# Kernel tuning notes

Hardware: AMD Instinct MI355X
Metric: run time of the kernel (lower is better)

Reference implementation:

```python
import jax, jax.numpy as jnp
import numpy as np

B, T, N, DIN, H, E, K, HM, CH, HOR, DOUT = 64, 12, 307, 1, 64, 10, 2, 16, 14, 12, 1
EPS = 1e-12


def setup_inputs() -> dict:
    key = jax.random.key(0)
    ks = jax.random.split(key, 16)
    rn = lambda k, s, sc=0.1: jax.random.normal(k, s, dtype=jnp.float32) * sc
    return {
        "hyper_source": jax.random.normal(ks[0], (B, CH, T, N), dtype=jnp.float32),
        "source": jax.random.normal(ks[1], (B, T, N, DIN), dtype=jnp.float32),
        "adj": jax.random.uniform(ks[2], (N, N), dtype=jnp.float32),
        "node_embeddings": rn(ks[3], (N, E), 1.0),
        "main_weights_pool": rn(ks[4], (E, H, DIN)),
        "hyper_W": rn(ks[5], (CH, H)),
        "hyper_b": jnp.zeros((H,), jnp.float32),
        "mask_W1": rn(ks[6], (H, HM)),
        "mask_W2": rn(ks[7], (HM, E)),
        "gate_Wpool": rn(ks[8], (E, K, 2 * DIN + H, 2 * H)),
        "gate_bpool": rn(ks[9], (E, 2 * H)),
        "upd_Wpool": rn(ks[10], (E, K, 2 * DIN + H, H)),
        "upd_bpool": rn(ks[11], (E, H)),
        "ln_gamma": jnp.ones((H,), jnp.float32),
        "ln_beta": jnp.zeros((H,), jnp.float32),
        "end_W": rn(ks[12], (HOR * DOUT, H)),
        "end_b": jnp.zeros((HOR * DOUT,), jnp.float32),
    }


def _forward(hyper_source, source, adj, node_embeddings, main_weights_pool,
             hyper_W, hyper_b, mask_W1, mask_W2, gate_Wpool, gate_bpool,
             upd_Wpool, upd_bpool, ln_gamma, ln_beta, end_W, end_b):
    # HyperNet: chunked long-history signal -> per-node per-step hidden h [B,N,T,H]
    h = jnp.tanh(jnp.einsum('bctn,ch->bnth', hyper_source, hyper_W) + hyper_b)
    # adaptive input channel: einsum('bnld,ndi->blni') with per-node weights
    weights_h = jnp.einsum('nd,dhi->nhi', node_embeddings, main_weights_pool)  # [N,H,DIN]
    x_adapt = jnp.einsum('bnlh,nhi->blni', h, weights_h)                       # [B,T,N,DIN]
    x = jnp.concatenate([x_adapt, source], axis=-1)                            # [B,T,N,2*DIN]
    # static Chebyshev supports (cheb_k=2): identity + mix(normalized adj, adaptive graph)
    adj_n = adj / jnp.clip(adj.sum(-1, keepdims=True), 1e-6)
    adapt = jax.nn.softmax(jax.nn.relu(node_embeddings @ node_embeddings.T), axis=1)
    A = 0.5 * (adj_n + adapt)
    supports = jnp.stack([jnp.eye(N, dtype=x.dtype), A])                       # [K,N,N]
    # per-node graph-conv weights generated from node embeddings
    gate_W = jnp.einsum('nd,dkio->nkio', node_embeddings, gate_Wpool)
    gate_b = node_embeddings @ gate_bpool
    upd_W = jnp.einsum('nd,dkio->nkio', node_embeddings, upd_Wpool)
    upd_b = node_embeddings @ upd_bpool

    def gconv(sup_b, xin, Wn, bn):
        xg = jnp.einsum('bknm,bmi->bnki', sup_b, xin)
        return jnp.einsum('bnki,nkio->bno', xg, Wn) + bn

    def step(state, inp):
        xt, ht = inp  # [B,N,2*DIN], [B,N,H]
        # dynamic graph sparsification mask from hypernet state
        logits = jnp.einsum('bne,me->bnm', (ht @ mask_W1) @ mask_W2, node_embeddings)
        mask = jax.nn.sigmoid(logits)                # [B,N,N]
        sup_b = supports[None] * mask[:, None]       # [B,K,N,N]
        xs = jnp.concatenate([xt, state], axis=-1)
        zr = jax.nn.sigmoid(gconv(sup_b, xs, gate_W, gate_b))
        z, r = jnp.split(zr, 2, axis=-1)
        cand = jnp.concatenate([xt, z * state], axis=-1)
        hc = jnp.tanh(gconv(sup_b, cand, upd_W, upd_b))
        return r * state + (1.0 - r) * hc, None

    init = jnp.zeros((x.shape[0], N, H), x.dtype)
    state, _ = jax.lax.scan(step, init,
                            (jnp.swapaxes(x, 0, 1), jnp.transpose(h, (2, 0, 1, 3))))
    # layernorm(eps=1e-12); dropout is identity at eval
    mu = state.mean(-1, keepdims=True)
    var = ((state - mu) ** 2).mean(-1, keepdims=True)
    xn = (state - mu) / jnp.sqrt(var + EPS) * ln_gamma + ln_beta
    # end_conv: Conv2d(1, HOR*DOUT, kernel=(1,H)) == per-node linear H -> HOR*DOUT
    out = jnp.einsum('bnh,oh->bon', xn, end_W) + end_b[None, :, None]
    out = out.reshape(-1, HOR, DOUT, N).transpose(0, 1, 3, 2)  # [B,HOR,N,DOUT]
    return out


def reference(hyper_source, source, adj, node_embeddings, main_weights_pool,
              hyper_W, hyper_b, mask_W1, mask_W2, gate_Wpool, gate_bpool,
              upd_Wpool, upd_bpool, ln_gamma, ln_beta, end_W, end_b):
    return _forward(hyper_source, source, adj, node_embeddings, main_weights_pool,
                    hyper_W, hyper_b, mask_W1, mask_W2, gate_Wpool, gate_bpool,
                    upd_Wpool, upd_bpool, ln_gamma, ln_beta, end_W, end_b)
```

## Files before the change

kernel.cpp:

```cpp
#include <hip/hip_runtime.h>
#include <hip/hip_bf16.h>

#define N_ 307
#define B_ 64
#define T_ 12
#define H_ 64
#define E_ 10
#define CH_ 14
#define HM_ 16
#define I2_ 66
#define GO_ 128
#define UO_ 64
#define QG_ (2 * I2_ * GO_)
#define QU_ (2 * I2_ * UO_)
#define TBN_ (T_ * B_ * N_)

__device__ __forceinline__ float wsum(float v) {
    #pragma unroll
    for (int off = 32; off; off >>= 1) v += __shfl_xor(v, off);
    return v;
}
__device__ __forceinline__ float wmax(float v) {
    #pragma unroll
    for (int off = 32; off; off >>= 1) v = fmaxf(v, __shfl_xor(v, off));
    return v;
}
__device__ __forceinline__ float sigm(float x) { return 1.f / (1.f + __expf(-x)); }
__device__ __forceinline__ float ftanh(float x) { return 1.f - 2.f / (__expf(2.f * x) + 1.f); }
__device__ __forceinline__ float bcast(float v, int l) {
    return __int_as_float(__builtin_amdgcn_readlane(__float_as_int(v), l));
}

__global__ void A_kernel(const float* __restrict__ adj, const float* __restrict__ nemb,
                         float* __restrict__ A) {
    const int n = blockIdx.x;
    const int lane = threadIdx.x;
    float en[E_];
    #pragma unroll
    for (int d = 0; d < E_; ++d) en[d] = nemb[n * E_ + d];
    float asum = 0.f;
    for (int m = lane; m < N_; m += 64) asum += adj[n * N_ + m];
    asum = fmaxf(wsum(asum), 1e-6f);
    float g[5]; bool valid[5];
    float mx = -1e30f;
    #pragma unroll
    for (int it = 0; it < 5; ++it) {
        int m = lane + it * 64;
        valid[it] = (m < N_);
        float dt = 0.f;
        if (valid[it]) {
            #pragma unroll
            for (int e = 0; e < E_; ++e) dt += en[e] * nemb[m * E_ + e];
            dt = fmaxf(dt, 0.f);
            mx = fmaxf(mx, dt);
        }
        g[it] = dt;
    }
    mx = wmax(mx);
    float se = 0.f;
    #pragma unroll
    for (int it = 0; it < 5; ++it)
        if (valid[it]) { g[it] = __expf(g[it] - mx); se += g[it]; }
    se = wsum(se);
    float inv = 1.f / se;
    #pragma unroll
    for (int it = 0; it < 5; ++it) {
        int m = lane + it * 64;
        if (valid[it]) A[n * N_ + m] = 0.5f * (adj[n * N_ + m] / asum + g[it] * inv);
    }
}

__device__ __forceinline__ float embdot(const float* __restrict__ nemb, int n,
                                        const float* __restrict__ pool, int Q, int q) {
    float a = 0.f;
    #pragma unroll
    for (int d = 0; d < E_; ++d) a += nemb[n * E_ + d] * pool[d * Q + q];
    return a;
}

__global__ __launch_bounds__(256) void gen_kernel(
    const float* __restrict__ nemb,
    const float* __restrict__ gWp, const float* __restrict__ gbp,
    const float* __restrict__ uWp, const float* __restrict__ ubp,
    const float* __restrict__ mwp,
    const float* __restrict__ W1, const float* __restrict__ W2,
    float* __restrict__ gW, float* __restrict__ gb,
    float* __restrict__ uW, float* __restrict__ ub,
    float* __restrict__ wh_t, float* __restrict__ W12) {
    const int e0 = N_ * QG_;
    const int e1 = e0 + N_ * GO_;
    const int e2 = e1 + N_ * QU_;
    const int e3 = e2 + N_ * UO_;
    const int e4 = e3 + N_ * H_;
    const int e5 = e4 + H_ * E_;
    int idx = blockIdx.x * 256 + threadIdx.x;
    if (idx < e0) {
        int n = idx / QG_, q = idx % QG_;
        gW[idx] = embdot(nemb, n, gWp, QG_, q);
    } else if (idx < e1) {
        int i = idx - e0; int n = i / GO_, q = i % GO_;
        gb[i] = embdot(nemb, n, gbp, GO_, q);
    } else if (idx < e2) {
        int i = idx - e1; int n = i / QU_, q = i % QU_;
        uW[i] = embdot(nemb, n, uWp, QU_, q);
    } else if (idx < e3) {
        int i = idx - e2; int n = i / UO_, q = i % UO_;
        ub[i] = embdot(nemb, n, ubp, UO_, q);
    } else if (idx < e4) {
        int i = idx - e3; int n = i / H_, q = i % H_;
        wh_t[q * N_ + n] = embdot(nemb, n, mwp, H_, q);
    } else if (idx < e5) {
        int i = idx - e4; int j = i / E_, e = i % E_;
        float a = 0.f;
        #pragma unroll
        for (int q = 0; q < HM_; ++q) a += W1[j * HM_ + q] * W2[q * E_ + e];
        W12[i] = a;
    }
}

__global__ __launch_bounds__(256) void hyper2_kernel(
    const float* __restrict__ hs, const float* __restrict__ src,
    const float* __restrict__ hyper_W, const float* __restrict__ hyper_b,
    const float* __restrict__ wh_t, const float* __restrict__ W12,
    float* __restrict__ x0, float* __restrict__ x1, float* __restrict__ emb) {
    const int tb = blockIdx.y;
    const int t = tb / B_, b = tb % B_;
    const int n = blockIdx.x * 256 + threadIdx.x;
    const bool act = (n < N_);
    const int nc = act ? n : N_ - 1;
    float hsv[CH_];
    #pragma unroll
    for (int c = 0; c < CH_; ++c)
        hsv[c] = hs[((b * CH_ + c) * T_ + t) * N_ + nc];
    float ax0 = 0.f;
    float ae[E_] = {};
    #pragma unroll 8
    for (int j = 0; j < H_; ++j) {
        float hj = hyper_b[j];
        #pragma unroll
        for (int c = 0; c < CH_; ++c) hj = fmaf(hsv[c], hyper_W[c * H_ + j], hj);
        hj = ftanh(hj);
        ax0 = fmaf(hj, wh_t[j * N_ + nc], ax0);
        #pragma unroll
        for (int e = 0; e < E_; ++e) ae[e] = fmaf(hj, W12[j * E_ + e], ae[e]);
    }
    if (act) {
        const int tbn = tb * N_ + n;
        x0[tbn] = ax0;
        x1[tbn] = src[(b * T_ + t) * N_ + n];
        #pragma unroll
        for (int e = 0; e < E_; ++e) emb[e * TBN_ + tbn] = ae[e];
    }
}

__global__ __launch_bounds__(256) void wm_kernel(
    const float* __restrict__ A, const float* __restrict__ emb,
    const float* __restrict__ nemb, const float* __restrict__ x0,
    const float* __restrict__ x1, float* __restrict__ Wm,
    float* __restrict__ dmask, float* __restrict__ aggx, int t) {
    const int wid = __builtin_amdgcn_readfirstlane(blockIdx.x * 4 + (threadIdx.x >> 6));
    const int lane = threadIdx.x & 63;
    const int b = wid / N_;
    const int n = wid % N_;
    const int tbn = (t * B_ + b) * N_ + n;
    const int xb = tbn - n;
    float et[E_];
    #pragma unroll
    for (int d = 0; d < E_; ++d) et[d] = emb[(size_t)d * TBN_ + tbn];
    float* wr = Wm + (size_t)(b * N_ + n) * N_;
    float a0 = 0.f, a1 = 0.f;
    #pragma unroll
    for (int c = 0; c < 5; ++c) {
        int m = c * 64 + lane;
        bool v = (m < N_);
        int mc = v ? m : 0;
        float dt = 0.f;
        #pragma unroll
        for (int d = 0; d < E_; ++d) dt += et[d] * nemb[mc * E_ + d];
        float sg = sigm(dt);
        float w = v ? A[n * N_ + mc] * sg : 0.f;
        if (v) {
            wr[m] = w;
            if (m == n) dmask[tbn] = sg;
            a0 += w * x0[xb + mc];
            a1 += w * x1[xb + mc];
        }
    }
    a0 = wsum(a0);
    a1 = wsum(a1);
    if (lane == 0) {
        aggx[(size_t)tbn * 2] = a0;
        aggx[(size_t)tbn * 2 + 1] = a1;
    }
}

__global__ __launch_bounds__(512) void aggS_kernel(
    const float* __restrict__ Wm, const float* __restrict__ Sin,
    float* __restrict__ aggS) {
    __shared__ float s_lds[N_ * 64];
    const int tid = threadIdx.x;
    const int lane = tid & 63;
    const int wv = tid >> 6;
    const int b = blockIdx.y;
    const int nb = blockIdx.x * 32 + wv * 4;
    {
        const float4* s4 = (const float4*)(Sin + (size_t)b * N_ * 64);
        float4* d4 = (float4*)s_lds;
        for (int idx = tid; idx < N_ * 16; idx += 512) d4[idx] = s4[idx];
    }
    __syncthreads();
    int roff[4];
    #pragma unroll
    for (int r = 0; r < 4; ++r) {
        int nr = nb + r; if (nr > N_ - 1) nr = N_ - 1;
        roff[r] = __builtin_amdgcn_readfirstlane((b * N_ + nr) * N_);
    }
    float acc[4] = {0.f, 0.f, 0.f, 0.f};
    #pragma unroll
    for (int ck = 0; ck < 4; ++ck) {
        const int m0 = ck << 6;
        float w0 = Wm[roff[0] + m0 + lane];
        float w1 = Wm[roff[1] + m0 + lane];
        float w2 = Wm[roff[2] + m0 + lane];
        float w3 = Wm[roff[3] + m0 + lane];
        #pragma unroll 8
        for (int mm = 0; mm < 64; ++mm) {
            float sv = s_lds[(m0 + mm) * 64 + lane];
            acc[0] = fmaf(bcast(w0, mm), sv, acc[0]);
            acc[1] = fmaf(bcast(w1, mm), sv, acc[1]);
            acc[2] = fmaf(bcast(w2, mm), sv, acc[2]);
            acc[3] = fmaf(bcast(w3, mm), sv, acc[3]);
        }
    }
    {
        const int m0 = 256;
        bool v = (m0 + lane < N_);
        float w0 = v ? Wm[roff[0] + m0 + lane] : 0.f;
        float w1 = v ? Wm[roff[1] + m0 + lane] : 0.f;
        float w2 = v ? Wm[roff[2] + m0 + lane] : 0.f;
        float w3 = v ? Wm[roff[3] + m0 + lane] : 0.f;
        #pragma unroll 8
        for (int mm = 0; mm < 51; ++mm) {
            float sv = s_lds[(m0 + mm) * 64 + lane];
            acc[0] = fmaf(bcast(w0, mm), sv, acc[0]);
            acc[1] = fmaf(bcast(w1, mm), sv, acc[1]);
            acc[2] = fmaf(bcast(w2, mm), sv, acc[2]);
            acc[3] = fmaf(bcast(w3, mm), sv, acc[3]);
        }
    }
    #pragma unroll
    for (int r = 0; r < 4; ++r) {
        int nr = nb + r;
        if (nr < N_) aggS[((size_t)b * N_ + nr) * 64 + lane] = acc[r];
    }
}

__global__ __launch_bounds__(256) void gate_mm_kernel(
    const float* __restrict__ gate_W, const float* __restrict__ gate_b,
    const float* __restrict__ x0, const float* __restrict__ x1,
    const float* __restrict__ S, const float* __restrict__ dmask,
    const float* __restrict__ aggx, const float* __restrict__ aggS,
    float* __restrict__ zs, float* __restrict__ rbuf, int t) {
    __shared__ float W_s[132][64];
    __shared__ float xg_s[32][132];
    const int oh = blockIdx.x, bh = blockIdx.y, n = blockIdx.z;
    const int tid = threadIdx.x;
    for (int idx = tid; idx < 132 * 64; idx += 256) {
        int row = idx >> 6, op = idx & 63;
        int col = (op < 32) ? (oh * 32 + op) : (64 + oh * 32 + (op - 32));
        W_s[row][op] = gate_W[(n * 132 + row) * GO_ + col];
    }
    for (int idx = tid; idx < 32 * 132; idx += 256) {
        int bl = idx / 132, i = idx % 132;
        int b = bh * 32 + bl;
        int tb = (t * B_ + b) * N_ + n;
        float v;
        if (i < 66) {
            float xs = (i == 0) ? x0[tb] : (i == 1) ? x1[tb] : S[(b * N_ + n) * 64 + (i - 2)];
            v = dmask[tb] * xs;
        } else {
            int i2 = i - 66;
            v = (i2 < 2) ? aggx[(size_t)tb * 2 + i2] : aggS[(b * N_ + n) * 64 + (i2 - 2)];
        }
        xg_s[bl][i] = v;
    }
    __syncthreads();
    const int bl = tid >> 3, og = tid & 7;
    float acc[8] = {};
    for (int i = 0; i < 132; ++i) {
        float xv = xg_s[bl][i];
        #pragma unroll
        for (int r = 0; r < 8; ++r) acc[r] += xv * W_s[i][og * 8 + r];
    }
    float v[8];
    #pragma unroll
    for (int r = 0; r < 8; ++r) {
        int op = og * 8 + r;
        int col = (op < 32) ? (oh * 32 + op) : (64 + oh * 32 + (op - 32));
        v[r] = sigm(acc[r] + gate_b[n * GO_ + col]);
    }
    __syncthreads();
    float* zr_s = &xg_s[0][0];
    #pragma unroll
    for (int r = 0; r < 8; ++r) zr_s[bl * 64 + og * 8 + r] = v[r];
    __syncthreads();
    for (int idx = tid; idx < 32 * 32; idx += 256) {
        int bl2 = idx >> 5, jl = idx & 31;
        int b = bh * 32 + bl2;
        int j = oh * 32 + jl;
        float z = zr_s[bl2 * 64 + jl];
        float rr = zr_s[bl2 * 64 + 32 + jl];
        int sidx = (b * N_ + n) * 64 + j;
        zs[sidx] = z * S[sidx];
        rbuf[sidx] = rr;
    }
}

__global__ __launch_bounds__(256) void upd_mm_kernel(
    const float* __restrict__ upd_W, const float* __restrict__ upd_b,
    const float* __restrict__ x0, const float* __restrict__ x1,
    const float* __restrict__ zsrc, const float* __restrict__ dmask,
    const float* __restrict__ aggx, const float* __restrict__ aggS,
    const float* __restrict__ rbuf, float* __restrict__ S, int t) {
    __shared__ float W_s[132][64];
    __shared__ float xg_s[32][132];
    const int bh = blockIdx.x, n = blockIdx.y;
    const int tid = threadIdx.x;
    for (int idx = tid; idx < 132 * 64; idx += 256) {
        int row = idx >> 6, op = idx & 63;
        W_s[row][op] = upd_W[(n * 132 + row) * UO_ + op];
    }
    for (int idx = tid; idx < 32 * 132; idx += 256) {
        int bl = idx / 132, i = idx % 132;
        int b = bh * 32 + bl;
        int tb = (t * B_ + b) * N_ + n;
        float v;
        if (i < 66) {
            float xs = (i == 0) ? x0[tb] : (i == 1) ? x1[tb] : zsrc[(b * N_ + n) * 64 + (i - 2)];
            v = dmask[tb] * xs;
        } else {
            int i2 = i - 66;
            v = (i2 < 2) ? aggx[(size_t)tb * 2 + i2] : aggS[(b * N_ + n) * 64 + (i2 - 2)];
        }
        xg_s[bl][i] = v;
    }
    __syncthreads();
    const int bl = tid >> 3, og = tid & 7;
    float acc[8] = {};
    for (int i = 0; i < 132; ++i) {
        float xv = xg_s[bl][i];
        #pragma unroll
        for (int r = 0; r < 8; ++r) acc[r] += xv * W_s[i][og * 8 + r];
    }
    const int b = bh * 32 + bl;
    #pragma unroll
    for (int r = 0; r < 8; ++r) {
        int op = og * 8 + r;
        float hc = ftanh(acc[r] + upd_b[n * UO_ + op]);
        int sidx = (b * N_ + n) * 64 + op;
        float rr = rbuf[sidx];
        float sv = S[sidx];
        S[sidx] = rr * sv + (1.f - rr) * hc;
    }
}

__global__ __launch_bounds__(256) void final_kernel(
    const float* __restrict__ S, const float* __restrict__ gamma,
    const float* __restrict__ beta, const float* __restrict__ endW,
    const float* __restrict__ endb, float* __restrict__ out) {
    const int wid = blockIdx.x * 4 + (threadIdx.x >> 6);
    const int lane = threadIdx.x & 63;
    const int b = wid / N_, n = wid % N_;
    float s = S[wid * 64 + lane];
    float mu = wsum(s) * (1.f / 64.f);
    float d = s - mu;
    float var = wsum(d * d) * (1.f / 64.f);
    float xn = d / sqrtf(var + 1e-12f) * gamma[lane] + beta[lane];
    #pragma unroll
    for (int o = 0; o < 12; ++o) {
        float dot = wsum(xn * endW[o * 64 + lane]);
        if (lane == o) out[(b * 12 + o) * N_ + n] = dot + endb[o];
    }
}

extern "C" void kernel_launch(void* const* d_in, const int* in_sizes, int n_in,
                              void* d_out, int out_size, void* d_ws, size_t ws_size,
                              hipStream_t stream) {
    const float* hyper_source = (const float*)d_in[0];
    const float* source       = (const float*)d_in[1];
    const float* adj          = (const float*)d_in[2];
    const float* nemb         = (const float*)d_in[3];
    const float* mwpool       = (const float*)d_in[4];
    const float* hyper_W      = (const float*)d_in[5];
    const float* hyper_b      = (const float*)d_in[6];
    const float* mask_W1      = (const float*)d_in[7];
    const float* mask_W2      = (const float*)d_in[8];
    const float* gate_Wpool   = (const float*)d_in[9];
    const float* gate_bpool   = (const float*)d_in[10];
    const float* upd_Wpool    = (const float*)d_in[11];
    const float* upd_bpool    = (const float*)d_in[12];
    const float* ln_gamma     = (const float*)d_in[13];
    const float* ln_beta      = (const float*)d_in[14];
    const float* end_W        = (const float*)d_in[15];
    const float* end_b        = (const float*)d_in[16];
    float* out = (float*)d_out;

    float* ws = (float*)d_ws;
    size_t off = 0;
    auto alloc = [&](size_t nf) {
        float* p = ws + off;
        off += (nf + 255) & ~(size_t)255;
        return p;
    };
    float* A      = alloc((size_t)N_ * N_);
    float* wh_t   = alloc((size_t)N_ * H_);
    float* W12    = alloc((size_t)H_ * E_);
    float* gate_W = alloc((size_t)N_ * QG_);
    float* gate_b = alloc((size_t)N_ * GO_);
    float* upd_W  = alloc((size_t)N_ * QU_);
    float* upd_b  = alloc((size_t)N_ * UO_);
    float* x0     = alloc((size_t)TBN_);
    float* x1     = alloc((size_t)TBN_);
    float* emb    = alloc((size_t)TBN_ * E_);
    float* dmask  = alloc((size_t)TBN_);
    float* aggx   = alloc((size_t)TBN_ * 2);
    float* S      = alloc((size_t)B_ * N_ * H_);
    float* zs     = alloc((size_t)B_ * N_ * H_);
    float* rbuf   = alloc((size_t)B_ * N_ * H_);
    float* aggS   = alloc((size_t)B_ * N_ * H_);
    float* Wm     = alloc((size_t)B_ * N_ * N_);

    hipMemsetAsync(S, 0, (size_t)B_ * N_ * H_ * sizeof(float), stream);

    A_kernel<<<N_, 64, 0, stream>>>(adj, nemb, A);

    const int gen_total = N_ * QG_ + N_ * GO_ + N_ * QU_ + N_ * UO_ + N_ * H_ + H_ * E_;
    gen_kernel<<<(gen_total + 255) / 256, 256, 0, stream>>>(
        nemb, gate_Wpool, gate_bpool, upd_Wpool, upd_bpool, mwpool, mask_W1, mask_W2,
        gate_W, gate_b, upd_W, upd_b, wh_t, W12);

    hyper2_kernel<<<dim3(2, T_ * B_), 256, 0, stream>>>(hyper_source, source, hyper_W,
                                                        hyper_b, wh_t, W12, x0, x1, emb);

    for (int t = 0; t < T_; ++t) {
        wm_kernel<<<(B_ * N_) / 4, 256, 0, stream>>>(A, emb, nemb, x0, x1, Wm, dmask, aggx, t);
        aggS_kernel<<<dim3(10, B_), 512, 0, stream>>>(Wm, S, aggS);
        gate_mm_kernel<<<dim3(2, 2, N_), 256, 0, stream>>>(gate_W, gate_b, x0, x1, S, dmask,
                                                           aggx, aggS, zs, rbuf, t);
        aggS_kernel<<<dim3(10, B_), 512, 0, stream>>>(Wm, zs, aggS);
        upd_mm_kernel<<<dim3(2, N_), 256, 0, stream>>>(upd_W, upd_b, x0, x1, zs, dmask, aggx,
                                                       aggS, rbuf, S, t);
    }

    final_kernel<<<(B_ * N_) / 4, 256, 0, stream>>>(S, ln_gamma, ln_beta, end_W, end_b, out);
}
```

Baseline: 2.303 ms.

## Store mask-weighted graph matrix in bf16 and retile aggregation and gate/update matmuls

After: 2.623 ms. 13.9% more time.

```diff
diff --git a/kernel.cpp b/kernel.cpp
--- a/kernel.cpp
+++ b/kernel.cpp
@@ -14,6 +14,7 @@
 #define QG_ (2 * I2_ * GO_)
 #define QU_ (2 * I2_ * UO_)
 #define TBN_ (T_ * B_ * N_)
+#define WMP_ 320
 
 __device__ __forceinline__ float wsum(float v) {
     #pragma unroll
@@ -29,6 +30,14 @@
 __device__ __forceinline__ float ftanh(float x) { return 1.f - 2.f / (__expf(2.f * x) + 1.f); }
 __device__ __forceinline__ float bcast(float v, int l) {
     return __int_as_float(__builtin_amdgcn_readlane(__float_as_int(v), l));
+}
+__device__ __forceinline__ unsigned short f2bf(float f) {
+    unsigned u = __float_as_uint(f);
+    u += 0x7FFFu + ((u >> 16) & 1u);
+    return (unsigned short)(u >> 16);
+}
+__device__ __forceinline__ float bf2f(unsigned short s) {
+    return __uint_as_float((unsigned)s << 16);
 }
 
 __global__ void A_kernel(const float* __restrict__ adj, const float* __restrict__ nemb,
@@ -156,7 +165,7 @@
 __global__ __launch_bounds__(256) void wm_kernel(
     const float* __restrict__ A, const float* __restrict__ emb,
     const float* __restrict__ nemb, const float* __restrict__ x0,
-    const float* __restrict__ x1, float* __restrict__ Wm,
+    const float* __restrict__ x1, unsigned short* __restrict__ Wm,
     float* __restrict__ dmask, float* __restrict__ aggx, int t) {
     const int wid = __builtin_amdgcn_readfirstlane(blockIdx.x * 4 + (threadIdx.x >> 6));
     const int lane = threadIdx.x & 63;
@@ -167,7 +176,7 @@
     float et[E_];
     #pragma unroll
     for (int d = 0; d < E_; ++d) et[d] = emb[(size_t)d * TBN_ + tbn];
-    float* wr = Wm + (size_t)(b * N_ + n) * N_;
+    unsigned short* wr = Wm + (size_t)(b * N_ + n) * WMP_;
     float a0 = 0.f, a1 = 0.f;
     #pragma unroll
     for (int c = 0; c < 5; ++c) {
@@ -179,8 +188,8 @@
         for (int d = 0; d < E_; ++d) dt += et[d] * nemb[mc * E_ + d];
         float sg = sigm(dt);
         float w = v ? A[n * N_ + mc] * sg : 0.f;
+        wr[m] = v ? f2bf(w) : (unsigned short)0;
         if (v) {
-            wr[m] = w;
             if (m == n) dmask[tbn] = sg;
             a0 += w * x0[xb + mc];
             a1 += w * x1[xb + mc];
@@ -195,57 +204,48 @@
 }
 
 __global__ __launch_bounds__(512) void aggS_kernel(
-    const float* __restrict__ Wm, const float* __restrict__ Sin,
+    const unsigned short* __restrict__ Wm, const float* __restrict__ Sin,
     float* __restrict__ aggS) {
-    __shared__ float s_lds[N_ * 64];
+    __shared__ float s_lds[128 * 64];
     const int tid = threadIdx.x;
     const int lane = tid & 63;
     const int wv = tid >> 6;
     const int b = blockIdx.y;
     const int nb = blockIdx.x * 32 + wv * 4;
-    {
-        const float4* s4 = (const float4*)(Sin + (size_t)b * N_ * 64);
-        float4* d4 = (float4*)s_lds;
-        for (int idx = tid; idx < N_ * 16; idx += 512) d4[idx] = s4[idx];
-    }
-    __syncthreads();
     int roff[4];
     #pragma unroll
     for (int r = 0; r < 4; ++r) {
         int nr = nb + r; if (nr > N_ - 1) nr = N_ - 1;
-        roff[r] = __builtin_amdgcn_readfirstlane((b * N_ + nr) * N_);
+        roff[r] = __builtin_amdgcn_readfirstlane((b * N_ + nr) * WMP_);
     }
     float acc[4] = {0.f, 0.f, 0.f, 0.f};
-    #pragma unroll
-    for (int ck = 0; ck < 4; ++ck) {
-        const int m0 = ck << 6;
-        float w0 = Wm[roff[0] + m0 + lane];
-        float w1 = Wm[roff[1] + m0 + lane];
-        float w2 = Wm[roff[2] + m0 + lane];
-        float w3 = Wm[roff[3] + m0 + lane];
-        #pragma unroll 8
-        for (int mm = 0; mm < 64; ++mm) {
-            float sv = s_lds[(m0 + mm) * 64 + lane];
-            acc[0] = fmaf(bcast(w0, mm), sv, acc[0]);
-            acc[1] = fmaf(bcast(w1, mm), sv, acc[1]);
-            acc[2] = fmaf(bcast(w2, mm), sv, acc[2]);
-            acc[3] = fmaf(bcast(w3, mm), sv, acc[3]);
-        }
-    }
-    {
-        const int m0 = 256;
-        bool v = (m0 + lane < N_);
-        float w0 = v ? Wm[roff[0] + m0 + lane] : 0.f;
-        float w1 = v ? Wm[roff[1] + m0 + lane] : 0.f;
-        float w2 = v ? Wm[roff[2] + m0 + lane] : 0.f;
-        float w3 = v ? Wm[roff[3] + m0 + lane] : 0.f;
-        #pragma unroll 8
-        for (int mm = 0; mm < 51; ++mm) {
-            float sv = s_lds[(m0 + mm) * 64 + lane];
-            acc[0] = fmaf(bcast(w0, mm), sv, acc[0]);
-            acc[1] = fmaf(bcast(w1, mm), sv, acc[1]);
-            acc[2] = fmaf(bcast(w2, mm), sv, acc[2]);
-            acc[3] = fmaf(bcast(w3, mm), sv, acc[3]);
+    const float4* s4 = (const float4*)(Sin + (size_t)b * N_ * 64);
+    float4* d4 = (float4*)s_lds;
+    #pragma unroll
+    for (int sck = 0; sck < 3; ++sck) {
+        const int mbase = sck * 128;
+        const int nrows = (sck < 2) ? 128 : 64;
+        if (sck) __syncthreads();
+        for (int idx = tid; idx < nrows * 16; idx += 512) {
+            int row = mbase + (idx >> 4);
+            int rc = (row < N_) ? row : N_ - 1;
+            d4[idx] = s4[rc * 16 + (idx & 15)];
+        }
+        __syncthreads();
+        for (int sub = 0; sub < nrows; sub += 64) {
+            const int m0 = mbase + sub;
+            float wf0 = bf2f(Wm[roff[0] + m0 + lane]);
+            float wf1 = bf2f(Wm[roff[1] + m0 + lane]);
+            float wf2 = bf2f(Wm[roff[2] + m0 + lane]);
+            float wf3 = bf2f(Wm[roff[3] + m0 + lane]);
+            #pragma unroll 8
+            for (int mm = 0; mm < 64; ++mm) {
+                float sv = s_lds[(sub + mm) * 64 + lane];
+                acc[0] = fmaf(bcast(wf0, mm), sv, acc[0]);
+                acc[1] = fmaf(bcast(wf1, mm), sv, acc[1]);
+                acc[2] = fmaf(bcast(wf2, mm), sv, acc[2]);
+                acc[3] = fmaf(bcast(wf3, mm), sv, acc[3]);
+            }
         }
     }
     #pragma unroll
@@ -262,17 +262,16 @@
     const float* __restrict__ aggx, const float* __restrict__ aggS,
     float* __restrict__ zs, float* __restrict__ rbuf, int t) {
     __shared__ float W_s[132][64];
-    __shared__ float xg_s[32][132];
-    const int oh = blockIdx.x, bh = blockIdx.y, n = blockIdx.z;
+    __shared__ float xg_s[64][132];
+    const int oh = blockIdx.x, n = blockIdx.y;
     const int tid = threadIdx.x;
     for (int idx = tid; idx < 132 * 64; idx += 256) {
         int row = idx >> 6, op = idx & 63;
         int col = (op < 32) ? (oh * 32 + op) : (64 + oh * 32 + (op - 32));
         W_s[row][op] = gate_W[(n * 132 + row) * GO_ + col];
     }
-    for (int idx = tid; idx < 32 * 132; idx += 256) {
-        int bl = idx / 132, i = idx % 132;
-        int b = bh * 32 + bl;
+    for (int idx = tid; idx < 64 * 132; idx += 256) {
+        int b = idx / 132, i = idx % 132;
         int tb = (t * B_ + b) * N_ + n;
         float v;
         if (i < 66) {
@@ -282,34 +281,37 @@
             int i2 = i - 66;
             v = (i2 < 2) ? aggx[(size_t)tb * 2 + i2] : aggS[(b * N_ + n) * 64 + (i2 - 2)];
         }
-        xg_s[bl][i] = v;
+        xg_s[b][i] = v;
     }
     __syncthreads();
-    const int bl = tid >> 3, og = tid & 7;
-    float acc[8] = {};
+    const int bl = (tid >> 3) * 2, og = tid & 7;
+    float acc[2][8] = {};
     for (int i = 0; i < 132; ++i) {
-        float xv = xg_s[bl][i];
-        #pragma unroll
-        for (int r = 0; r < 8; ++r) acc[r] += xv * W_s[i][og * 8 + r];
-    }
-    float v[8];
-    #pragma unroll
-    for (int r = 0; r < 8; ++r) {
-        int op = og * 8 + r;
-        int col = (op < 32) ? (oh * 32 + op) : (64 + oh * 32 + (op - 32));
-        v[r] = sigm(acc[r] + gate_b[n * GO_ + col]);
+        float xv0 = xg_s[bl][i], xv1 = xg_s[bl + 1][i];
+        #pragma unroll
+        for (int r = 0; r < 8; ++r) {
+            float wv = W_s[i][og * 8 + r];
+            acc[0][r] = fmaf(xv0, wv, acc[0][r]);
+            acc[1][r] = fmaf(xv1, wv, acc[1][r]);
+        }
     }
     __syncthreads();
     float* zr_s = &xg_s[0][0];
     #pragma unroll
-    for (int r = 0; r < 8; ++r) zr_s[bl * 64 + og * 8 + r] = v[r];
+    for (int q = 0; q < 2; ++q) {
+        #pragma unroll
+        for (int r = 0; r < 8; ++r) {
+            int op = og * 8 + r;
+            int col = (op < 32) ? (oh * 32 + op) : (64 + oh * 32 + (op - 32));
+            zr_s[(bl + q) * 64 + op] = sigm(acc[q][r] + gate_b[n * GO_ + col]);
+        }
+    }
     __syncthreads();
-    for (int idx = tid; idx < 32 * 32; idx += 256) {
-        int bl2 = idx >> 5, jl = idx & 31;
-        int b = bh * 32 + bl2;
+    for (int idx = tid; idx < 64 * 32; idx += 256) {
+        int b = idx >> 5, jl = idx & 31;
         int j = oh * 32 + jl;
-        float z = zr_s[bl2 * 64 + jl];
-        float rr = zr_s[bl2 * 64 + 32 + jl];
+        float z = zr_s[b * 64 + jl];
+        float rr = zr_s[b * 64 + 32 + jl];
         int sidx = (b * N_ + n) * 64 + j;
         zs[sidx] = z * S[sidx];
         rbuf[sidx] = rr;
@@ -323,16 +325,15 @@
     const float* __restrict__ aggx, const float* __restrict__ aggS,
     const float* __restrict__ rbuf, float* __restrict__ S, int t) {
     __shared__ float W_s[132][64];
-    __shared__ float xg_s[32][132];
-    const int bh = blockIdx.x, n = blockIdx.y;
+    __shared__ float xg_s[64][132];
+    const int n = blockIdx.x;
     const int tid = threadIdx.x;
     for (int idx = tid; idx < 132 * 64; idx += 256) {
         int row = idx >> 6, op = idx & 63;
         W_s[row][op] = upd_W[(n * 132 + row) * UO_ + op];
     }
-    for (int idx = tid; idx < 32 * 132; idx += 256) {
-        int bl = idx / 132, i = idx % 132;
-        int b = bh * 32 + bl;
+    for (int idx = tid; idx < 64 * 132; idx += 256) {
+        int b = idx / 132, i = idx % 132;
         int tb = (t * B_ + b) * N_ + n;
         float v;
         if (i < 66) {
@@ -342,25 +343,32 @@
             int i2 = i - 66;
             v = (i2 < 2) ? aggx[(size_t)tb * 2 + i2] : aggS[(b * N_ + n) * 64 + (i2 - 2)];
         }
-        xg_s[bl][i] = v;
+        xg_s[b][i] = v;
     }
     __syncthreads();
-    const int bl = tid >> 3, og = tid & 7;
-    float acc[8] = {};
+    const int bl = (tid >> 3) * 2, og = tid & 7;
+    float acc[2][8] = {};
     for (int i = 0; i < 132; ++i) {
-        float xv = xg_s[bl][i];
-        #pragma unroll
-        for (int r = 0; r < 8; ++r) acc[r] += xv * W_s[i][og * 8 + r];
-    }
-    const int b = bh * 32 + bl;
-    #pragma unroll
-    for (int r = 0; r < 8; ++r) {
-        int op = og * 8 + r;
-        float hc = ftanh(acc[r] + upd_b[n * UO_ + op]);
-        int sidx = (b * N_ + n) * 64 + op;
-        float rr = rbuf[sidx];
-        float sv = S[sidx];
-        S[sidx] = rr * sv + (1.f - rr) * hc;
+        float xv0 = xg_s[bl][i], xv1 = xg_s[bl + 1][i];
+        #pragma unroll
+        for (int r = 0; r < 8; ++r) {
+            float wv = W_s[i][og * 8 + r];
+            acc[0][r] = fmaf(xv0, wv, acc[0][r]);
+            acc[1][r] = fmaf(xv1, wv, acc[1][r]);
+        }
+    }
+    #pragma unroll
+    for (int q = 0; q < 2; ++q) {
+        int b = bl + q;
+        #pragma unroll
+        for (int r = 0; r < 8; ++r) {
+            int op = og * 8 + r;
+            float hc = ftanh(acc[q][r] + upd_b[n * UO_ + op]);
+            int sidx = (b * N_ + n) * 64 + op;
+            float rr = rbuf[sidx];
+            float sv = S[sidx];
+            S[sidx] = rr * sv + (1.f - rr) * hc;
+        }
     }
 }
 
@@ -428,7 +436,7 @@
     float* zs     = alloc((size_t)B_ * N_ * H_);
     float* rbuf   = alloc((size_t)B_ * N_ * H_);
     float* aggS   = alloc((size_t)B_ * N_ * H_);
-    float* Wm     = alloc((size_t)B_ * N_ * N_);
+    unsigned short* Wm = (unsigned short*)alloc((size_t)B_ * N_ * WMP_ / 2);
 
     hipMemsetAsync(S, 0, (size_t)B_ * N_ * H_ * sizeof(float), stream);
 
@@ -445,11 +453,11 @@
     for (int t = 0; t < T_; ++t) {
         wm_kernel<<<(B_ * N_) / 4, 256, 0, stream>>>(A, emb, nemb, x0, x1, Wm, dmask, aggx, t);
         aggS_kernel<<<dim3(10, B_), 512, 0, stream>>>(Wm, S, aggS);
-        gate_mm_kernel<<<dim3(2, 2, N_), 256, 0, stream>>>(gate_W, gate_b, x0, x1, S, dmask,
-                                                           aggx, aggS, zs, rbuf, t);
+        gate_mm_kernel<<<dim3(2, N_), 256, 0, stream>>>(gate_W, gate_b, x0, x1, S, dmask,
+                                                        aggx, aggS, zs, rbuf, t);
         aggS_kernel<<<dim3(10, B_), 512, 0, stream>>>(Wm, zs, aggS);
-        upd_mm_kernel<<<dim3(2, N_), 256, 0, stream>>>(upd_W, upd_b, x0, x1, zs, dmask, aggx,
-                                                       aggS, rbuf, S, t);
+        upd_mm_kernel<<<N_, 256, 0, stream>>>(upd_W, upd_b, x0, x1, zs, dmask, aggx,
+                                              aggS, rbuf, S, t);
     }
 
     final_kernel<<<(B_ * N_) / 4, 256, 0, stream>>>(S, ln_gamma, ln_beta, end_W, end_b, out);
```
